# Optimization experiments

Hardware: AMD Instinct MI355X
Metric: run time of the kernel (lower is better)

## Reference

```python
import jax, jax.numpy as jnp
import numpy as np

D = 1024
H = 16
HD = D // H
MLP = 4 * D


def _lin(key, fin, fout):
    k1, k2 = jax.random.split(key)
    lim = 1.0 / np.sqrt(fin)
    W = jax.random.uniform(k1, (fin, fout), minval=-lim, maxval=lim, dtype=jnp.float32)
    b = jax.random.uniform(k2, (fout,), minval=-lim, maxval=lim, dtype=jnp.float32)
    return W, b


def setup_inputs() -> dict:
    key = jax.random.key(0)
    ks = jax.random.split(key, 10)
    x = jax.random.normal(ks[0], (4, 2048, D), dtype=jnp.float32)
    time_emb = jax.random.normal(ks[1], (4, D), dtype=jnp.float32)
    Wqkv, bqkv = _lin(ks[2], D, 3 * D)
    Wproj, bproj = _lin(ks[3], D, D)
    W1, b1 = _lin(ks[4], D, MLP)
    W2, b2 = _lin(ks[5], MLP, D)
    Wt, bt = _lin(ks[6], D, 6 * D)
    g1 = jnp.ones((D,), jnp.float32); be1 = jnp.zeros((D,), jnp.float32)
    g2 = jnp.ones((D,), jnp.float32); be2 = jnp.zeros((D,), jnp.float32)
    return {"x": x, "time_emb": time_emb, "Wqkv": Wqkv, "bqkv": bqkv,
            "Wproj": Wproj, "bproj": bproj, "W1": W1, "b1": b1, "W2": W2, "b2": b2,
            "Wt": Wt, "bt": bt, "g1": g1, "be1": be1, "g2": g2, "be2": be2}


def layernorm(x, g, b, eps=1e-5):
    mu = jnp.mean(x, axis=-1, keepdims=True)
    var = jnp.var(x, axis=-1, keepdims=True)
    return (x - mu) * jax.lax.rsqrt(var + eps) * g + b


def attention(h, Wqkv, bqkv, Wproj, bproj):
    B, L, _ = h.shape
    qkv = (h @ Wqkv + bqkv).reshape(B, L, 3, H, HD)
    q, k, v = jnp.moveaxis(qkv, 2, 0)  # each [B,L,H,HD]
    scale = HD ** -0.5
    attn = jnp.einsum('blhd,bmhd->bhlm', q, k) * scale
    attn = jax.nn.softmax(attn, axis=-1)
    out = jnp.einsum('bhlm,bmhd->blhd', attn, v).reshape(B, L, D)
    return out @ Wproj + bproj


def reference(x, time_emb, Wqkv, bqkv, Wproj, bproj, W1, b1, W2, b2, Wt, bt, g1, be1, g2, be2):
    tp = (jax.nn.silu(time_emb) @ Wt + bt)[:, None, :]  # [B,1,6D]
    shift_msa, scale_msa, gate_msa, shift_mlp, scale_mlp, gate_mlp = jnp.split(tp, 6, axis=-1)
    h = layernorm(x, g1, be1)
    h = h * (1.0 + scale_msa) + shift_msa
    h = attention(h, Wqkv, bqkv, Wproj, bproj)
    x = x + gate_msa * h
    h = layernorm(x, g2, be2)
    h = h * (1.0 + scale_mlp) + shift_mlp
    h = jax.nn.gelu(h @ W1 + b1, approximate=False) @ W2 + b2
    x = x + gate_mlp * h
    return x
```

## Files before the change

kernel.cpp:

```cpp
#include <hip/hip_runtime.h>
#include <hip/hip_bf16.h>
#include <math.h>


typedef __attribute__((ext_vector_type(8))) __bf16 bf16x8;
typedef __attribute__((ext_vector_type(4))) float f32x4;

union FragU { uint4 u; bf16x8 b; };

#define AS1(p) ((const __attribute__((address_space(1))) void*)(p))
#define AS3(p) ((__attribute__((address_space(3))) void*)(p))

__device__ __forceinline__ float bflo(uint u) {
    union { uint i; float f; } v; v.i = u << 16; return v.f;
}
__device__ __forceinline__ ushort f2bf(float f) {
    union { float f; uint i; } v; v.f = f;
    uint r = (v.i + 0x7fffu + ((v.i >> 16) & 1u)) >> 16;
    return (ushort)r;
}
__device__ __forceinline__ uint pkbf(float a, float b) {
    return __builtin_amdgcn_perm(__float_as_uint(b), __float_as_uint(a), 0x07060302u);
}
__device__ __forceinline__ void stval(ushort* p, float v) { *p = f2bf(v); }
__device__ __forceinline__ void stval(float* p, float v) { *p = v; }

__global__ __launch_bounds__(256) void transpose_f2b(const float* __restrict__ in,
                                                     ushort* __restrict__ out,
                                                     int R, int C) {
    __shared__ ushort t[32][33];
    int c0 = blockIdx.x * 32, r0 = blockIdx.y * 32;
    int tx = threadIdx.x, ty = threadIdx.y;
#pragma unroll
    for (int i = 0; i < 32; i += 8)
        t[ty + i][tx] = f2bf(in[(size_t)(r0 + ty + i) * C + c0 + tx]);
    __syncthreads();
#pragma unroll
    for (int i = 0; i < 32; i += 8)
        out[(size_t)(c0 + ty + i) * R + r0 + tx] = t[tx][ty + i];
}

__global__ __launch_bounds__(256) void tp_gemm(const float* __restrict__ te,
                                               const ushort* __restrict__ WtT,
                                               const float* __restrict__ bt,
                                               float* __restrict__ tp) {
    int w = blockIdx.x * 4 + (threadIdx.x >> 6);
    int lane = threadIdx.x & 63;
    int b = w / 6144, n = w % 6144;
    const ushort* wr = WtT + (size_t)n * 1024;
    const float* tr = te + (size_t)b * 1024;
    float s = 0.f;
#pragma unroll
    for (int i = 0; i < 16; i++) {
        int k = lane + 64 * i;
        float t = tr[k];
        float sil = t / (1.f + __expf(-t));
        s += sil * bflo((uint)wr[k]);
    }
#pragma unroll
    for (int x = 32; x; x >>= 1) s += __shfl_xor(s, x);
    if (lane == 0) tp[(size_t)b * 6144 + n] = s + bt[n];
}

__global__ __launch_bounds__(256) void ln_mod(const float* __restrict__ x,
                                              const float* __restrict__ tpb,
                                              const float* __restrict__ g,
                                              const float* __restrict__ be,
                                              ushort* __restrict__ out,
                                              int shift_off, int scale_off) {
    __shared__ float2 sred[4];
    int row = blockIdx.x;
    int b = row >> 11;
    int tid = threadIdx.x;
    float4 f = *(const float4*)&x[(size_t)row * 1024 + tid * 4];
    float v[4] = {f.x, f.y, f.z, f.w};
    float s = v[0] + v[1] + v[2] + v[3];
    float s2 = v[0] * v[0] + v[1] * v[1] + v[2] * v[2] + v[3] * v[3];
#pragma unroll
    for (int m = 32; m; m >>= 1) { s += __shfl_xor(s, m); s2 += __shfl_xor(s2, m); }
    if ((tid & 63) == 0) sred[tid >> 6] = make_float2(s, s2);
    __syncthreads();
    s = sred[0].x + sred[1].x + sred[2].x + sred[3].x;
    s2 = sred[0].y + sred[1].y + sred[2].y + sred[3].y;
    float mu = s * (1.f / 1024.f);
    float var = s2 * (1.f / 1024.f) - mu * mu;
    float rs = rsqrtf(var + 1e-5f);
    const float* tprow = tpb + (size_t)b * 6144;
    ushort o4[4];
#pragma unroll
    for (int t = 0; t < 4; t++) {
        int c = tid * 4 + t;
        float y = (v[t] - mu) * rs * g[c] + be[c];
        y = y * (1.f + tprow[scale_off + c]) + tprow[shift_off + c];
        o4[t] = f2bf(y);
    }
    *(uint2*)&out[(size_t)row * 1024 + tid * 4] = *(uint2*)o4;
}

template <int EPI, typename OT>
__global__ __launch_bounds__(256) void gemm_bt(const ushort* __restrict__ A,
                                               const ushort* __restrict__ BT,
                                               const float* __restrict__ bias,
                                               OT* __restrict__ C,
                                               int M, int N, int K,
                                               const float* __restrict__ res,
                                               const float* __restrict__ tpb,
                                               int goff) {
    __shared__ __align__(16) ushort As[128 * 32];
    __shared__ __align__(16) ushort Bs[128 * 32];
    int m0 = blockIdx.y * 128, n0 = blockIdx.x * 128;
    int tid = threadIdx.x;
    int wid = tid >> 6, lane = tid & 63;
    int wy = wid >> 1, wx = wid & 1;
    int r16 = lane & 15;
    int q8 = (lane >> 4) << 3;

    f32x4 acc[4][4];
#pragma unroll
    for (int i = 0; i < 4; i++)
#pragma unroll
        for (int j = 0; j < 4; j++) acc[i][j] = (f32x4){0.f, 0.f, 0.f, 0.f};

    int sr = tid >> 2;
    int sc = (tid & 3) << 3;
    const ushort* Abase = A + (size_t)(m0 + sr) * K + sc;
    const ushort* Bbase = BT + (size_t)(n0 + sr) * K + sc;
    ushort* AsW = As + (size_t)wid * 512;
    ushort* BsW = Bs + (size_t)wid * 512;

    for (int k0 = 0; k0 < K; k0 += 32) {
        __builtin_amdgcn_global_load_lds(AS1(Abase + k0), AS3(AsW), 16, 0, 0);
        __builtin_amdgcn_global_load_lds(AS1(Abase + (size_t)64 * K + k0), AS3(AsW + 2048), 16, 0, 0);
        __builtin_amdgcn_global_load_lds(AS1(Bbase + k0), AS3(BsW), 16, 0, 0);
        __builtin_amdgcn_global_load_lds(AS1(Bbase + (size_t)64 * K + k0), AS3(BsW + 2048), 16, 0, 0);
        __syncthreads();
        FragU fa[4], fb[4];
#pragma unroll
        for (int i = 0; i < 4; i++)
            fa[i].u = *(const uint4*)&As[(wy * 64 + i * 16 + r16) * 32 + q8];
#pragma unroll
        for (int j = 0; j < 4; j++)
            fb[j].u = *(const uint4*)&Bs[(wx * 64 + j * 16 + r16) * 32 + q8];
#pragma unroll
        for (int i = 0; i < 4; i++)
#pragma unroll
            for (int j = 0; j < 4; j++)
                acc[i][j] = __builtin_amdgcn_mfma_f32_16x16x32_bf16(fa[i].b, fb[j].b, acc[i][j], 0, 0, 0);
        __syncthreads();
    }

    int q4 = (lane >> 4) << 2;
#pragma unroll
    for (int i = 0; i < 4; i++) {
#pragma unroll
        for (int j = 0; j < 4; j++) {
            int col = n0 + wx * 64 + j * 16 + r16;
            float bv = bias[col];
#pragma unroll
            for (int t = 0; t < 4; t++) {
                int row = m0 + wy * 64 + i * 16 + q4 + t;
                float v = acc[i][j][t] + bv;
                if constexpr (EPI == 1) {
                    v = 0.5f * v * (1.f + erff(v * 0.70710678118f));
                }
                if constexpr (EPI == 2) {
                    float rv = res[(size_t)row * N + col];
                    float gate = tpb[(size_t)(row >> 11) * 6144 + goff + col];
                    v = rv + gate * v;
                }
                stval(&C[(size_t)row * N + col], v);
            }
        }
    }
}

__global__ __launch_bounds__(256, 4) void attn_mfma(const ushort* __restrict__ qkv,
                                                    ushort* __restrict__ out) {
    __shared__ __align__(16) ushort Ks[64 * 72];
    __shared__ __align__(16) ushort Vs[64 * 72];
    __shared__ __align__(16) ushort Ps[64 * 72];

    int tid = threadIdx.x;
    int wid = tid >> 6, lane = tid & 63;
    int r16 = lane & 15, quad = lane >> 4;
    int q8 = quad << 3, q4 = quad << 2;

    int bh = blockIdx.x >> 5;
    int qt = blockIdx.x & 31;
    int b = bh >> 4, h = bh & 15;
    const ushort* qkbase = qkv + (size_t)b * 2048 * 3072 + h * 64;

    {
        int r = tid >> 2;
        int c = (tid & 3) << 4;
        const ushort* qp = qkbase + (size_t)(qt * 64 + r) * 3072 + c;
        *(uint4*)&Ps[r * 72 + c] = *(const uint4*)qp;
        *(uint4*)&Ps[r * 72 + c + 8] = *(const uint4*)(qp + 8);
    }
    __syncthreads();
    FragU qa[2];
#pragma unroll
    for (int ks = 0; ks < 2; ks++)
        qa[ks].u = *(const uint4*)&Ps[(wid * 16 + r16) * 72 + ks * 32 + q8];

    float m_ = -1e30f, l_ = 0.f;
    f32x4 o[4];
#pragma unroll
    for (int dn = 0; dn < 4; dn++) o[dn] = (f32x4){0.f, 0.f, 0.f, 0.f};

    int kr = tid >> 2;
    int kc = (tid & 3) << 4;
    int vk = (tid & 31) << 1;
    int vd = (tid >> 5) << 3;
    const ushort* kptr = qkbase + 1024 + (size_t)kr * 3072 + kc;
    const ushort* vptr = qkbase + 2048 + (size_t)vk * 3072 + vd;

    uint4 ka0 = *(const uint4*)kptr;
    uint4 ka1 = *(const uint4*)(kptr + 8);
    uint4 va0 = *(const uint4*)vptr;
    uint4 va1 = *(const uint4*)(vptr + 3072);

    for (int kt = 0; kt < 32; kt++) {
        __syncthreads();
        *(uint4*)&Ks[kr * 72 + kc] = ka0;
        *(uint4*)&Ks[kr * 72 + kc + 8] = ka1;
        *(uint*)&Vs[(vd + 0) * 72 + vk] = (va0.x & 0xffffu) | (va1.x << 16);
        *(uint*)&Vs[(vd + 1) * 72 + vk] = (va0.x >> 16) | (va1.x & 0xffff0000u);
        *(uint*)&Vs[(vd + 2) * 72 + vk] = (va0.y & 0xffffu) | (va1.y << 16);
        *(uint*)&Vs[(vd + 3) * 72 + vk] = (va0.y >> 16) | (va1.y & 0xffff0000u);
        *(uint*)&Vs[(vd + 4) * 72 + vk] = (va0.z & 0xffffu) | (va1.z << 16);
        *(uint*)&Vs[(vd + 5) * 72 + vk] = (va0.z >> 16) | (va1.z & 0xffff0000u);
        *(uint*)&Vs[(vd + 6) * 72 + vk] = (va0.w & 0xffffu) | (va1.w << 16);
        *(uint*)&Vs[(vd + 7) * 72 + vk] = (va0.w >> 16) | (va1.w & 0xffff0000u);
        __syncthreads();

        if (kt < 31) {
            const ushort* kp2 = kptr + (size_t)(kt + 1) * 64 * 3072;
            const ushort* vp2 = vptr + (size_t)(kt + 1) * 64 * 3072;
            ka0 = *(const uint4*)kp2;
            ka1 = *(const uint4*)(kp2 + 8);
            va0 = *(const uint4*)vp2;
            va1 = *(const uint4*)(vp2 + 3072);
        }

        f32x4 s[4];
#pragma unroll
        for (int n = 0; n < 4; n++) s[n] = (f32x4){0.f, 0.f, 0.f, 0.f};
#pragma unroll
        for (int ks = 0; ks < 2; ks++) {
            FragU kb[4];
#pragma unroll
            for (int n = 0; n < 4; n++)
                kb[n].u = *(const uint4*)&Ks[(n * 16 + r16) * 72 + ks * 32 + q8];
#pragma unroll
            for (int n = 0; n < 4; n++)
                s[n] = __builtin_amdgcn_mfma_f32_16x16x32_bf16(kb[n].b, qa[ks].b, s[n], 0, 0, 0);
        }

        float mx = fmaxf(fmaxf(fmaxf(s[0][0], s[0][1]), fmaxf(s[0][2], s[0][3])),
                         fmaxf(fmaxf(s[1][0], s[1][1]), fmaxf(s[1][2], s[1][3])));
        mx = fmaxf(mx, fmaxf(fmaxf(fmaxf(s[2][0], s[2][1]), fmaxf(s[2][2], s[2][3])),
                             fmaxf(fmaxf(s[3][0], s[3][1]), fmaxf(s[3][2], s[3][3]))));
        mx = fmaxf(mx, __shfl_xor(mx, 16));
        mx = fmaxf(mx, __shfl_xor(mx, 32));
        float nm = fmaxf(m_, mx);
        float al = __expf((m_ - nm) * 0.125f);
        float cc = nm * 0.125f;
        m_ = nm;

        float p[4][4];
        float ps = 0.f;
#pragma unroll
        for (int n = 0; n < 4; n++)
#pragma unroll
            for (int t = 0; t < 4; t++) {
                p[n][t] = __expf(__fmaf_rn(s[n][t], 0.125f, -cc));
                ps += p[n][t];
            }
        ps += __shfl_xor(ps, 16);
        ps += __shfl_xor(ps, 32);
        l_ = l_ * al + ps;
#pragma unroll
        for (int dn = 0; dn < 4; dn++)
#pragma unroll
            for (int t = 0; t < 4; t++) o[dn][t] *= al;

#pragma unroll
        for (int n = 0; n < 4; n++) {
            uint2 w2 = make_uint2(pkbf(p[n][0], p[n][1]), pkbf(p[n][2], p[n][3]));
            *(uint2*)&Ps[(wid * 16 + r16) * 72 + n * 16 + q4] = w2;
        }

#pragma unroll
        for (int ks = 0; ks < 2; ks++) {
            FragU pa, vb[4];
            pa.u = *(const uint4*)&Ps[(wid * 16 + r16) * 72 + ks * 32 + q8];
#pragma unroll
            for (int dn = 0; dn < 4; dn++)
                vb[dn].u = *(const uint4*)&Vs[(dn * 16 + r16) * 72 + ks * 32 + q8];
#pragma unroll
            for (int dn = 0; dn < 4; dn++)
                o[dn] = __builtin_amdgcn_mfma_f32_16x16x32_bf16(vb[dn].b, pa.b, o[dn], 0, 0, 0);
        }
    }

    float inv = 1.f / l_;
    int row = qt * 64 + wid * 16 + r16;
    ushort* orow = out + (size_t)(b * 2048 + row) * 1024 + h * 64;
#pragma unroll
    for (int dn = 0; dn < 4; dn++) {
        uint2 w2 = make_uint2(pkbf(o[dn][0] * inv, o[dn][1] * inv),
                              pkbf(o[dn][2] * inv, o[dn][3] * inv));
        *(uint2*)&orow[dn * 16 + q4] = w2;
    }
}

extern "C" void kernel_launch(void* const* d_in, const int* in_sizes, int n_in,
                              void* d_out, int out_size, void* d_ws, size_t ws_size,
                              hipStream_t stream) {
    const float* x    = (const float*)d_in[0];
    const float* te   = (const float*)d_in[1];
    const float* Wqkv = (const float*)d_in[2];
    const float* bqkv = (const float*)d_in[3];
    const float* Wproj= (const float*)d_in[4];
    const float* bproj= (const float*)d_in[5];
    const float* W1   = (const float*)d_in[6];
    const float* b1   = (const float*)d_in[7];
    const float* W2   = (const float*)d_in[8];
    const float* b2   = (const float*)d_in[9];
    const float* Wt   = (const float*)d_in[10];
    const float* bt   = (const float*)d_in[11];
    const float* g1   = (const float*)d_in[12];
    const float* be1  = (const float*)d_in[13];
    const float* g2   = (const float*)d_in[14];
    const float* be2  = (const float*)d_in[15];

    char* ws = (char*)d_ws;
    ushort* WqkvT  = (ushort*)(ws + 0);
    ushort* WprojT = (ushort*)(ws + 6291456);
    ushort* W1T    = (ushort*)(ws + 8388608);
    ushort* W2T    = (ushort*)(ws + 16777216);
    ushort* WtT    = (ushort*)(ws + 25165824);
    float*  tpb    = (float*)(ws + 37748736);
    ushort* hbuf   = (ushort*)(ws + 37847040);
    ushort* qkvb   = (ushort*)(ws + 54624256);
    ushort* midb   = (ushort*)(ws + 54624256);
    ushort* attnb  = (ushort*)(ws + 121733120);
    float*  x1b    = (float*)(ws + 138510336);

    dim3 tb(32, 8);
    hipLaunchKernelGGL(transpose_f2b, dim3(3072 / 32, 1024 / 32), tb, 0, stream, Wqkv, WqkvT, 1024, 3072);
    hipLaunchKernelGGL(transpose_f2b, dim3(1024 / 32, 1024 / 32), tb, 0, stream, Wproj, WprojT, 1024, 1024);
    hipLaunchKernelGGL(transpose_f2b, dim3(4096 / 32, 1024 / 32), tb, 0, stream, W1, W1T, 1024, 4096);
    hipLaunchKernelGGL(transpose_f2b, dim3(1024 / 32, 4096 / 32), tb, 0, stream, W2, W2T, 4096, 1024);
    hipLaunchKernelGGL(transpose_f2b, dim3(6144 / 32, 1024 / 32), tb, 0, stream, Wt, WtT, 1024, 6144);

    hipLaunchKernelGGL(tp_gemm, dim3(6144), dim3(256), 0, stream, te, WtT, bt, tpb);

    hipLaunchKernelGGL(ln_mod, dim3(8192), dim3(256), 0, stream, x, tpb, g1, be1, hbuf, 0, 1024);

    hipLaunchKernelGGL((gemm_bt<0, ushort>), dim3(3072 / 128, 8192 / 128), dim3(256), 0, stream,
                       hbuf, WqkvT, bqkv, qkvb, 8192, 3072, 1024, (const float*)nullptr, (const float*)nullptr, 0);

    hipLaunchKernelGGL(attn_mfma, dim3(2048), dim3(256), 0, stream, qkvb, attnb);

    hipLaunchKernelGGL((gemm_bt<2, float>), dim3(1024 / 128, 8192 / 128), dim3(256), 0, stream,
                       attnb, WprojT, bproj, x1b, 8192, 1024, 1024, x, tpb, 2048);

    hipLaunchKernelGGL(ln_mod, dim3(8192), dim3(256), 0, stream, x1b, tpb, g2, be2, hbuf, 3072, 4096);

    hipLaunchKernelGGL((gemm_bt<1, ushort>), dim3(4096 / 128, 8192 / 128), dim3(256), 0, stream,
                       hbuf, W1T, b1, midb, 8192, 4096, 1024, (const float*)nullptr, (const float*)nullptr, 0);

    hipLaunchKernelGGL((gemm_bt<2, float>), dim3(1024 / 128, 8192 / 128), dim3(256), 0, stream,
                       midb, W2T, b2, (float*)d_out, 8192, 1024, 4096, x1b, tpb, 5120);
}
```

Baseline: 674.1 us.

## Pre-transpose V for attention and split-K the W2 GEMM with reduce

Adds a kernel that writes V transposed per head so the attention kernel loads V tiles with contiguous vector stores instead of per-element shuffles. The final MLP down-projection (K=4096) is split into two K halves, each written as bf16 partials over dead workspace regions, and a separate reduce kernel adds bias, gate and residual. The aim is more blocks for the narrow N=1024 GEMM and cheaper V staging. In exchange it adds two launches and extra memory traffic, and rounds the partial sums to bf16, which costs some precision.

```diff
diff --git a/kernel.cpp b/kernel.cpp
--- a/kernel.cpp
+++ b/kernel.cpp
@@ -13,6 +13,9 @@
 
 __device__ __forceinline__ float bflo(uint u) {
     union { uint i; float f; } v; v.i = u << 16; return v.f;
+}
+__device__ __forceinline__ float bfhi(uint u) {
+    union { uint i; float f; } v; v.i = u & 0xffff0000u; return v.f;
 }
 __device__ __forceinline__ ushort f2bf(float f) {
     union { float f; uint i; } v; v.f = f;
@@ -38,6 +41,22 @@
 #pragma unroll
     for (int i = 0; i < 32; i += 8)
         out[(size_t)(c0 + ty + i) * R + r0 + tx] = t[tx][ty + i];
+}
+
+__global__ __launch_bounds__(256) void transpose_v(const ushort* __restrict__ qkv,
+                                                   ushort* __restrict__ vT) {
+    int bh = blockIdx.x >> 5, lt = blockIdx.x & 31;
+    int b = bh >> 4, h = bh & 15;
+    int d = threadIdx.x & 63, lg = threadIdx.x >> 6;
+    const ushort* src = qkv + (size_t)b * 2048 * 3072 + 2048 + h * 64 + d;
+#pragma unroll
+    for (int g = 0; g < 2; g++) {
+        int l0 = lt * 64 + lg * 16 + g * 8;
+        ushort v[8];
+#pragma unroll
+        for (int i = 0; i < 8; i++) v[i] = src[(size_t)(l0 + i) * 3072];
+        *(uint4*)&vT[((size_t)bh * 64 + d) * 2048 + l0] = *(uint4*)v;
+    }
 }
 
 __global__ __launch_bounds__(256) void tp_gemm(const float* __restrict__ te,
@@ -174,7 +193,93 @@
     }
 }
 
+__global__ __launch_bounds__(256) void gemm_sk(const ushort* __restrict__ A,
+                                               const ushort* __restrict__ BT,
+                                               ushort* __restrict__ p0,
+                                               ushort* __restrict__ p1) {
+    __shared__ __align__(16) ushort As[128 * 32];
+    __shared__ __align__(16) ushort Bs[128 * 32];
+    int m0 = blockIdx.y * 128, n0 = blockIdx.x * 128;
+    int z = blockIdx.z;
+    int tid = threadIdx.x;
+    int wid = tid >> 6, lane = tid & 63;
+    int wy = wid >> 1, wx = wid & 1;
+    int r16 = lane & 15;
+    int q8 = (lane >> 4) << 3;
+
+    f32x4 acc[4][4];
+#pragma unroll
+    for (int i = 0; i < 4; i++)
+#pragma unroll
+        for (int j = 0; j < 4; j++) acc[i][j] = (f32x4){0.f, 0.f, 0.f, 0.f};
+
+    int sr = tid >> 2;
+    int sc = (tid & 3) << 3;
+    const ushort* Abase = A + (size_t)(m0 + sr) * 4096 + z * 2048 + sc;
+    const ushort* Bbase = BT + (size_t)(n0 + sr) * 4096 + z * 2048 + sc;
+    ushort* AsW = As + (size_t)wid * 512;
+    ushort* BsW = Bs + (size_t)wid * 512;
+
+    for (int k0 = 0; k0 < 2048; k0 += 32) {
+        __builtin_amdgcn_global_load_lds(AS1(Abase + k0), AS3(AsW), 16, 0, 0);
+        __builtin_amdgcn_global_load_lds(AS1(Abase + (size_t)64 * 4096 + k0), AS3(AsW + 2048), 16, 0, 0);
+        __builtin_amdgcn_global_load_lds(AS1(Bbase + k0), AS3(BsW), 16, 0, 0);
+        __builtin_amdgcn_global_load_lds(AS1(Bbase + (size_t)64 * 4096 + k0), AS3(BsW + 2048), 16, 0, 0);
+        __syncthreads();
+        FragU fa[4], fb[4];
+#pragma unroll
+        for (int i = 0; i < 4; i++)
+            fa[i].u = *(const uint4*)&As[(wy * 64 + i * 16 + r16) * 32 + q8];
+#pragma unroll
+        for (int j = 0; j < 4; j++)
+            fb[j].u = *(const uint4*)&Bs[(wx * 64 + j * 16 + r16) * 32 + q8];
+#pragma unroll
+        for (int i = 0; i < 4; i++)
+#pragma unroll
+            for (int j = 0; j < 4; j++)
+                acc[i][j] = __builtin_amdgcn_mfma_f32_16x16x32_bf16(fa[i].b, fb[j].b, acc[i][j], 0, 0, 0);
+        __syncthreads();
+    }
+
+    ushort* P = z ? p1 : p0;
+    int q4 = (lane >> 4) << 2;
+#pragma unroll
+    for (int i = 0; i < 4; i++)
+#pragma unroll
+        for (int j = 0; j < 4; j++) {
+            int col = n0 + wx * 64 + j * 16 + r16;
+#pragma unroll
+            for (int t = 0; t < 4; t++) {
+                int row = m0 + wy * 64 + i * 16 + q4 + t;
+                P[(size_t)row * 1024 + col] = f2bf(acc[i][j][t]);
+            }
+        }
+}
+
+__global__ __launch_bounds__(256) void w2_reduce(const ushort* __restrict__ p0,
+                                                 const ushort* __restrict__ p1,
+                                                 const float* __restrict__ x1,
+                                                 const float* __restrict__ b2,
+                                                 const float* __restrict__ tpb,
+                                                 float* __restrict__ out) {
+    int row = blockIdx.x;
+    int b = row >> 11;
+    int c = threadIdx.x * 4;
+    size_t off = (size_t)row * 1024 + c;
+    uint2 u0 = *(const uint2*)&p0[off];
+    uint2 u1 = *(const uint2*)&p1[off];
+    float4 xr = *(const float4*)&x1[off];
+    const float* gp = tpb + (size_t)b * 6144 + 5120 + c;
+    float4 o;
+    o.x = xr.x + gp[0] * (bflo(u0.x) + bflo(u1.x) + b2[c + 0]);
+    o.y = xr.y + gp[1] * (bfhi(u0.x) + bfhi(u1.x) + b2[c + 1]);
+    o.z = xr.z + gp[2] * (bflo(u0.y) + bflo(u1.y) + b2[c + 2]);
+    o.w = xr.w + gp[3] * (bfhi(u0.y) + bfhi(u1.y) + b2[c + 3]);
+    *(float4*)&out[off] = o;
+}
+
 __global__ __launch_bounds__(256, 4) void attn_mfma(const ushort* __restrict__ qkv,
+                                                    const ushort* __restrict__ vT,
                                                     ushort* __restrict__ out) {
     __shared__ __align__(16) ushort Ks[64 * 72];
     __shared__ __align__(16) ushort Vs[64 * 72];
@@ -210,37 +315,29 @@
 
     int kr = tid >> 2;
     int kc = (tid & 3) << 4;
-    int vk = (tid & 31) << 1;
-    int vd = (tid >> 5) << 3;
     const ushort* kptr = qkbase + 1024 + (size_t)kr * 3072 + kc;
-    const ushort* vptr = qkbase + 2048 + (size_t)vk * 3072 + vd;
+    const ushort* vptr = vT + (size_t)bh * 131072 + (size_t)kr * 2048 + kc;
 
     uint4 ka0 = *(const uint4*)kptr;
     uint4 ka1 = *(const uint4*)(kptr + 8);
     uint4 va0 = *(const uint4*)vptr;
-    uint4 va1 = *(const uint4*)(vptr + 3072);
+    uint4 va1 = *(const uint4*)(vptr + 8);
 
     for (int kt = 0; kt < 32; kt++) {
         __syncthreads();
         *(uint4*)&Ks[kr * 72 + kc] = ka0;
         *(uint4*)&Ks[kr * 72 + kc + 8] = ka1;
-        *(uint*)&Vs[(vd + 0) * 72 + vk] = (va0.x & 0xffffu) | (va1.x << 16);
-        *(uint*)&Vs[(vd + 1) * 72 + vk] = (va0.x >> 16) | (va1.x & 0xffff0000u);
-        *(uint*)&Vs[(vd + 2) * 72 + vk] = (va0.y & 0xffffu) | (va1.y << 16);
-        *(uint*)&Vs[(vd + 3) * 72 + vk] = (va0.y >> 16) | (va1.y & 0xffff0000u);
-        *(uint*)&Vs[(vd + 4) * 72 + vk] = (va0.z & 0xffffu) | (va1.z << 16);
-        *(uint*)&Vs[(vd + 5) * 72 + vk] = (va0.z >> 16) | (va1.z & 0xffff0000u);
-        *(uint*)&Vs[(vd + 6) * 72 + vk] = (va0.w & 0xffffu) | (va1.w << 16);
-        *(uint*)&Vs[(vd + 7) * 72 + vk] = (va0.w >> 16) | (va1.w & 0xffff0000u);
+        *(uint4*)&Vs[kr * 72 + kc] = va0;
+        *(uint4*)&Vs[kr * 72 + kc + 8] = va1;
         __syncthreads();
 
         if (kt < 31) {
             const ushort* kp2 = kptr + (size_t)(kt + 1) * 64 * 3072;
-            const ushort* vp2 = vptr + (size_t)(kt + 1) * 64 * 3072;
+            const ushort* vp2 = vptr + (kt + 1) * 64;
             ka0 = *(const uint4*)kp2;
             ka1 = *(const uint4*)(kp2 + 8);
             va0 = *(const uint4*)vp2;
-            va1 = *(const uint4*)(vp2 + 3072);
+            va1 = *(const uint4*)(vp2 + 8);
         }
 
         f32x4 s[4];
@@ -343,10 +440,13 @@
     ushort* WtT    = (ushort*)(ws + 25165824);
     float*  tpb    = (float*)(ws + 37748736);
     ushort* hbuf   = (ushort*)(ws + 37847040);
+    ushort* vTb    = (ushort*)(ws + 37847040);
     ushort* qkvb   = (ushort*)(ws + 54624256);
     ushort* midb   = (ushort*)(ws + 54624256);
     ushort* attnb  = (ushort*)(ws + 121733120);
     float*  x1b    = (float*)(ws + 138510336);
+    ushort* p0b    = (ushort*)(ws + 0);
+    ushort* p1b    = (ushort*)(ws + 37847040);
 
     dim3 tb(32, 8);
     hipLaunchKernelGGL(transpose_f2b, dim3(3072 / 32, 1024 / 32), tb, 0, stream, Wqkv, WqkvT, 1024, 3072);
@@ -362,7 +462,9 @@
     hipLaunchKernelGGL((gemm_bt<0, ushort>), dim3(3072 / 128, 8192 / 128), dim3(256), 0, stream,
                        hbuf, WqkvT, bqkv, qkvb, 8192, 3072, 1024, (const float*)nullptr, (const float*)nullptr, 0);
 
-    hipLaunchKernelGGL(attn_mfma, dim3(2048), dim3(256), 0, stream, qkvb, attnb);
+    hipLaunchKernelGGL(transpose_v, dim3(2048), dim3(256), 0, stream, qkvb, vTb);
+
+    hipLaunchKernelGGL(attn_mfma, dim3(2048), dim3(256), 0, stream, qkvb, vTb, attnb);
 
     hipLaunchKernelGGL((gemm_bt<2, float>), dim3(1024 / 128, 8192 / 128), dim3(256), 0, stream,
                        attnb, WprojT, bproj, x1b, 8192, 1024, 1024, x, tpb, 2048);
@@ -372,6 +474,6 @@
     hipLaunchKernelGGL((gemm_bt<1, ushort>), dim3(4096 / 128, 8192 / 128), dim3(256), 0, stream,
                        hbuf, W1T, b1, midb, 8192, 4096, 1024, (const float*)nullptr, (const float*)nullptr, 0);
 
-    hipLaunchKernelGGL((gemm_bt<2, float>), dim3(1024 / 128, 8192 / 128), dim3(256), 0, stream,
-                       midb, W2T, b2, (float*)d_out, 8192, 1024, 4096, x1b, tpb, 5120);
-}
+    hipLaunchKernelGGL(gemm_sk, dim3(8, 64, 2), dim3(256), 0, stream, midb, W2T, p0b, p1b);
+    hipLaunchKernelGGL(w2_reduce, dim3(8192), dim3(256), 0, stream, p0b, p1b, x1b, b2, tpb, (float*)d_out);
+}
```

Result: no change. 680.9 us (+1.0%).
